# Optimization experiments

Measured on AMD Instinct MI355X. Metric: run time of the kernel, lower is better.

Reference implementation:

```python
import jax, jax.numpy as jnp
import numpy as np

N = 8192
IN_F = 256
OUT_F = 128


def setup_inputs() -> dict:
    key = jax.random.key(0)
    k1, k2, k3, k4, k5, k6 = jax.random.split(key, 6)
    input = jax.random.normal(k1, (N, IN_F), dtype=jnp.float32)
    adj = jax.random.randint(k2, (N, N), 0, 2, dtype=jnp.int32)
    # xavier-uniform-like init scaled by gain=0.5
    def xavier(k, shape, gain=0.5):
        fan_in, fan_out = shape[0], shape[1]
        lim = gain * np.sqrt(6.0 / (fan_in + fan_out))
        return jax.random.uniform(k, shape, dtype=jnp.float32, minval=-lim, maxval=lim)
    W_s = xavier(k3, (IN_F, OUT_F))
    a_s = xavier(k4, (OUT_F, 1))
    W_n = xavier(k5, (IN_F, OUT_F))
    a_n = xavier(k6, (OUT_F, 1))
    return {"input": input, "adj": adj, "W_s": W_s, "a_s": a_s, "W_n": W_n, "a_n": a_n}


def reference(input, adj, W_s, a_s, W_n, a_n):
    # Projections: [N, out_features]
    h_s = input @ W_s
    h_n = input @ W_n
    # Additive attention logits: e[i, j] = relu((h_s @ a_s)[i] + (h_n @ a_n)[j])
    e = jax.nn.relu((h_s @ a_s) + (h_n @ a_n).T)  # [N, N]
    # Masked softmax over neighbors (dim=1)
    attention = jnp.where(adj > 0, e, jnp.float32(-9e15))
    attention = jax.nn.softmax(attention, axis=1)
    # Self-scaling term (sum of softmax rows, kept for faithfulness)
    attention_sum = jnp.sum(attention, axis=-1, keepdims=True)
    attention_s = 1.0 / (1.0 + attention_sum)
    # Dropout is identity in eval mode (p=0 / training=False)
    h_prime = attention_s * h_s + attention @ h_n
    # concat=True -> elu activation
    return jax.nn.elu(h_prime)
```

## Files before the change

### kernel.cpp

```cpp
#include <hip/hip_runtime.h>
#include <math.h>

#define NN 8192

typedef short short8 __attribute__((ext_vector_type(8)));
typedef float f32x4 __attribute__((ext_vector_type(4)));

__device__ __forceinline__ float eluf(float x) {
  return x > 0.f ? x : (__expf(x) - 1.f);
}
__device__ __forceinline__ unsigned short f2bf(float f) {
  union { float f; unsigned u; } v; v.f = f;
  unsigned r = v.u + 0x7fffu + ((v.u >> 16) & 1u);
  return (unsigned short)(r >> 16);
}
__device__ __forceinline__ unsigned pack4(int4 v, int sh) {
  return ((unsigned)(v.x & 1) << sh) | ((unsigned)(v.y & 1) << (sh + 1)) |
         ((unsigned)(v.z & 1) << (sh + 2)) | ((unsigned)(v.w & 1) << (sh + 3));
}

__global__ __launch_bounds__(256) void k_proj(const float* __restrict__ X,
                                              const float* __restrict__ Ws,
                                              const float* __restrict__ Wn,
                                              const float* __restrict__ as_,
                                              const float* __restrict__ an_,
                                              float* __restrict__ Hs,
                                              unsigned short* __restrict__ HnT,
                                              float* __restrict__ es_out,
                                              float* __restrict__ en_out) {
  __shared__ float4 lin4[8 * 64];
  const int t = threadIdx.x;
  const int i0 = blockIdx.x * 8;
  const float4* Xg = (const float4*)X + (size_t)i0 * 64;
  lin4[t] = Xg[t];
  if (t < 256) lin4[t + 256] = Xg[t + 256];
  __syncthreads();
  const int c = t & 127;
  const int rh = t >> 7;
  float accs[4], accn[4];
#pragma unroll
  for (int r = 0; r < 4; ++r) { accs[r] = 0.f; accn[r] = 0.f; }
  for (int k = 0; k < 256; k += 4) {
    float ws0 = Ws[(k + 0) * 128 + c], ws1 = Ws[(k + 1) * 128 + c];
    float ws2 = Ws[(k + 2) * 128 + c], ws3 = Ws[(k + 3) * 128 + c];
    float wn0 = Wn[(k + 0) * 128 + c], wn1 = Wn[(k + 1) * 128 + c];
    float wn2 = Wn[(k + 2) * 128 + c], wn3 = Wn[(k + 3) * 128 + c];
#pragma unroll
    for (int r = 0; r < 4; ++r) {
      float4 iv = lin4[(rh * 4 + r) * 64 + (k >> 2)];
      accs[r] = fmaf(iv.x, ws0, accs[r]); accs[r] = fmaf(iv.y, ws1, accs[r]);
      accs[r] = fmaf(iv.z, ws2, accs[r]); accs[r] = fmaf(iv.w, ws3, accs[r]);
      accn[r] = fmaf(iv.x, wn0, accn[r]); accn[r] = fmaf(iv.y, wn1, accn[r]);
      accn[r] = fmaf(iv.z, wn2, accn[r]); accn[r] = fmaf(iv.w, wn3, accn[r]);
    }
  }
#pragma unroll
  for (int r = 0; r < 4; ++r)
    Hs[(size_t)(i0 + rh * 4 + r) * 128 + c] = accs[r];
  {
    union { unsigned short us[4]; ushort4 u4; } pk;
#pragma unroll
    for (int r = 0; r < 4; ++r) pk.us[r] = f2bf(accn[r]);
    *(ushort4*)(HnT + (size_t)blockIdx.x * 1024 + c * 8 + rh * 4) = pk.u4;
  }
  float* red = (float*)lin4;
  const int wv = t >> 6, ln = t & 63;
  __syncthreads();
  {
    float av = as_[c];
#pragma unroll
    for (int r = 0; r < 4; ++r) red[(rh * 4 + r) * 128 + c] = accs[r] * av;
  }
  __syncthreads();
#pragma unroll
  for (int h = 0; h < 2; ++h) {
    int row = wv * 2 + h;
    float p = red[row * 128 + ln] + red[row * 128 + 64 + ln];
#pragma unroll
    for (int off = 32; off >= 1; off >>= 1) p += __shfl_down(p, off);
    if (ln == 0) es_out[i0 + row] = __expf(p);
  }
  __syncthreads();
  {
    float av = an_[c];
#pragma unroll
    for (int r = 0; r < 4; ++r) red[(rh * 4 + r) * 128 + c] = accn[r] * av;
  }
  __syncthreads();
#pragma unroll
  for (int h = 0; h < 2; ++h) {
    int row = wv * 2 + h;
    float p = red[row * 128 + ln] + red[row * 128 + 64 + ln];
#pragma unroll
    for (int off = 32; off >= 1; off >>= 1) p += __shfl_down(p, off);
    if (ln == 0) en_out[i0 + row] = __expf(p);
  }
}

__global__ __launch_bounds__(512, 4) void k_main(const int* __restrict__ A,
                                                 const unsigned short* __restrict__ HnT,
                                                 const float* __restrict__ es_g,
                                                 const float* __restrict__ en_g,
                                                 float* __restrict__ HsOut) {
  __shared__ __align__(16) char smem[49152];
  float* en_lds = (float*)smem;
  unsigned* bits_lds = (unsigned*)(smem + 32768);
  float* cmb = (float*)smem;
  __shared__ float zsh[8][16];
  __shared__ float zf[16];

  const int t = threadIdx.x;
  const int wv = t >> 6;
  const int ln = t & 63;
  const int q = ln >> 4;
  const int m = ln & 15;
  const int row0 = blockIdx.x * 16;

  {
    float4* dst = (float4*)en_lds;
    const float4* s4 = (const float4*)en_g;
#pragma unroll
    for (int k = 0; k < 4; ++k) dst[t + k * 512] = s4[t + k * 512];
#pragma unroll 1
    for (int k = 0; k < 8; ++k) {
      int g = t + k * 512;
      int rr = g >> 8;
      int c8 = g & 255;
      const int4* src = (const int4*)(A + (size_t)(row0 + rr) * NN + c8 * 32);
      int4 v0 = src[0], v1 = src[1], v2 = src[2], v3 = src[3];
      int4 v4 = src[4], v5 = src[5], v6 = src[6], v7 = src[7];
      unsigned w = pack4(v0, 0)  | pack4(v1, 4)  | pack4(v2, 8)  | pack4(v3, 12) |
                   pack4(v4, 16) | pack4(v5, 20) | pack4(v6, 24) | pack4(v7, 28);
      bits_lds[(c8 >> 5) * 512 + (c8 & 31) * 16 + rr] = w;
    }
  }

  const float sme = es_g[row0 + m];
  const unsigned short* bptr = HnT + ((size_t)(wv * 128 + q) * 128 + m) * 8;
  const float* nvl = en_lds + wv * 1024 + q * 8;
  const unsigned* bts = bits_lds + wv * 512 + m;

  f32x4 acc[8];
#pragma unroll
  for (int ft = 0; ft < 8; ++ft) acc[ft] = (f32x4){0.f, 0.f, 0.f, 0.f};
  float zp = 0.f;

  union Breg { uint4 u; short8 s; };
  Breg breg[8];

  __syncthreads();

  breg[0].u = *(const uint4*)(bptr);       breg[1].u = *(const uint4*)(bptr + 128);
  breg[2].u = *(const uint4*)(bptr + 256); breg[3].u = *(const uint4*)(bptr + 384);
  breg[4].u = *(const uint4*)(bptr + 512); breg[5].u = *(const uint4*)(bptr + 640);
  breg[6].u = *(const uint4*)(bptr + 768); breg[7].u = *(const uint4*)(bptr + 896);

#pragma unroll 2
  for (int tt = 0; tt < 32; ++tt) {
    short8 fr;
    {
      float4 nv0 = *(const float4*)(nvl + tt * 32);
      float4 nv1 = *(const float4*)(nvl + tt * 32 + 4);
      const unsigned bw = bts[tt * 16];
      const unsigned byte = (bw >> (q * 8)) & 0xffu;
      float ev[8] = {nv0.x, nv0.y, nv0.z, nv0.w, nv1.x, nv1.y, nv1.z, nv1.w};
#pragma unroll
      for (int k = 0; k < 8; ++k) {
        float w = ((byte >> k) & 1u) ? fmaxf(sme * ev[k], 1.f) : 0.f;
        zp += w;
        fr[k] = (short)f2bf(w);
      }
    }
    __builtin_amdgcn_s_setprio(1);
    acc[0] = __builtin_amdgcn_mfma_f32_16x16x32_bf16(fr, breg[0].s, acc[0], 0, 0, 0);
    acc[1] = __builtin_amdgcn_mfma_f32_16x16x32_bf16(fr, breg[1].s, acc[1], 0, 0, 0);
    acc[2] = __builtin_amdgcn_mfma_f32_16x16x32_bf16(fr, breg[2].s, acc[2], 0, 0, 0);
    acc[3] = __builtin_amdgcn_mfma_f32_16x16x32_bf16(fr, breg[3].s, acc[3], 0, 0, 0);
    acc[4] = __builtin_amdgcn_mfma_f32_16x16x32_bf16(fr, breg[4].s, acc[4], 0, 0, 0);
    acc[5] = __builtin_amdgcn_mfma_f32_16x16x32_bf16(fr, breg[5].s, acc[5], 0, 0, 0);
    acc[6] = __builtin_amdgcn_mfma_f32_16x16x32_bf16(fr, breg[6].s, acc[6], 0, 0, 0);
    acc[7] = __builtin_amdgcn_mfma_f32_16x16x32_bf16(fr, breg[7].s, acc[7], 0, 0, 0);
    __builtin_amdgcn_s_setprio(0);
    {
      const unsigned short* p = bptr + (size_t)(tt + 1) * 4096;
      breg[0].u = *(const uint4*)(p);       breg[1].u = *(const uint4*)(p + 128);
      breg[2].u = *(const uint4*)(p + 256); breg[3].u = *(const uint4*)(p + 384);
      breg[4].u = *(const uint4*)(p + 512); breg[5].u = *(const uint4*)(p + 640);
      breg[6].u = *(const uint4*)(p + 768); breg[7].u = *(const uint4*)(p + 896);
    }
  }

  {
    float zz = zp;
    zz += __shfl_down(zz, 32);
    zz += __shfl_down(zz, 16);
    if (ln < 16) zsh[wv][ln] = zz;
  }
  __syncthreads();
  if (wv >= 4) {
#pragma unroll
    for (int ft = 0; ft < 8; ++ft)
#pragma unroll
      for (int reg = 0; reg < 4; ++reg)
        cmb[(wv - 4) * 2048 + (q * 4 + reg) * 128 + ft * 16 + m] = acc[ft][reg];
  }
  __syncthreads();
  if (wv < 4) {
#pragma unroll
    for (int ft = 0; ft < 8; ++ft)
#pragma unroll
      for (int reg = 0; reg < 4; ++reg)
        acc[ft][reg] += cmb[wv * 2048 + (q * 4 + reg) * 128 + ft * 16 + m];
  }
  __syncthreads();
  if (wv < 4) {
#pragma unroll
    for (int ft = 0; ft < 8; ++ft)
#pragma unroll
      for (int reg = 0; reg < 4; ++reg)
        cmb[wv * 2048 + (q * 4 + reg) * 128 + ft * 16 + m] = acc[ft][reg];
  }
  if (t < 16) {
    float z = zsh[0][t] + zsh[1][t] + zsh[2][t] + zsh[3][t] +
              zsh[4][t] + zsh[5][t] + zsh[6][t] + zsh[7][t];
    zf[t] = 1.f / z;
  }
  __syncthreads();
  {
    const int row = t >> 5;
    const int f0 = (t & 31) * 4;
    f32x4 ssum = *(const f32x4*)&cmb[row * 128 + f0];
#pragma unroll
    for (int w = 1; w < 4; ++w) ssum += *(const f32x4*)&cmb[w * 2048 + row * 128 + f0];
    const float invz = zf[row];
    const size_t off = (size_t)(row0 + row) * 128 + f0;
    float4 h = *(const float4*)(HsOut + off);
    float4 o;
    o.x = eluf(fmaf(ssum[0], invz, 0.5f * h.x));
    o.y = eluf(fmaf(ssum[1], invz, 0.5f * h.y));
    o.z = eluf(fmaf(ssum[2], invz, 0.5f * h.z));
    o.w = eluf(fmaf(ssum[3], invz, 0.5f * h.w));
    *(float4*)(HsOut + off) = o;
  }
}

extern "C" void kernel_launch(void* const* d_in, const int* in_sizes, int n_in,
                              void* d_out, int out_size, void* d_ws, size_t ws_size,
                              hipStream_t stream) {
  const float* X   = (const float*)d_in[0];
  const int*   A   = (const int*)d_in[1];
  const float* Ws  = (const float*)d_in[2];
  const float* as_ = (const float*)d_in[3];
  const float* Wn  = (const float*)d_in[4];
  const float* an_ = (const float*)d_in[5];
  float* out = (float*)d_out;

  unsigned short* HnT = (unsigned short*)d_ws;
  float* es = (float*)(HnT + (size_t)128 * NN);
  float* en = es + NN;

  k_proj<<<1024, 256, 0, stream>>>(X, Ws, Wn, as_, an_, out, HnT, es, en);
  k_main<<<512, 512, 0, stream>>>(A, HnT, es, en, out);
}
```

Baseline: 423.7 us.

## Pack adjacency bitmask in a separate pre-pass fused with projection kernel

Adjacency-to-bitmask packing moves from the attention kernel's prologue into the projection kernel, run as extra interleaved blocks that write a packed bit array to workspace. The main kernel then reads 32x less adjacency data per block before its compute loop. This removes the long serialized global-load prologue from each main block. The cost is an extra write and read of the packed mask and a larger first kernel.

Result: no change. 418.3 us (-1.3%).

```diff
diff --git a/kernel.cpp b/kernel.cpp
--- a/kernel.cpp
+++ b/kernel.cpp
@@ -19,21 +19,43 @@
          ((unsigned)(v.z & 1) << (sh + 2)) | ((unsigned)(v.w & 1) << (sh + 3));
 }
 
-__global__ __launch_bounds__(256) void k_proj(const float* __restrict__ X,
-                                              const float* __restrict__ Ws,
-                                              const float* __restrict__ Wn,
-                                              const float* __restrict__ as_,
-                                              const float* __restrict__ an_,
-                                              float* __restrict__ Hs,
-                                              unsigned short* __restrict__ HnT,
-                                              float* __restrict__ es_out,
-                                              float* __restrict__ en_out) {
+__global__ __launch_bounds__(256) void k_pre(const float* __restrict__ X,
+                                             const int* __restrict__ A,
+                                             const float* __restrict__ Ws,
+                                             const float* __restrict__ Wn,
+                                             const float* __restrict__ as_,
+                                             const float* __restrict__ an_,
+                                             float* __restrict__ Hs,
+                                             unsigned short* __restrict__ HnT,
+                                             float* __restrict__ es_out,
+                                             float* __restrict__ en_out,
+                                             unsigned* __restrict__ P) {
   __shared__ float4 lin4[8 * 64];
+  const int bid = blockIdx.x;
+  const int q5 = bid / 5, r5 = bid - q5 * 5;
   const int t = threadIdx.x;
-  const int i0 = blockIdx.x * 8;
+
+  if (r5 == 4) {
+    const int row0 = q5 * 32;
+#pragma unroll 1
+    for (int k = 0; k < 32; ++k) {
+      int g = t + k * 256;
+      int rr = g >> 8;
+      int c8 = g & 255;
+      const int4* src = (const int4*)(A + (size_t)(row0 + rr) * NN + c8 * 32);
+      int4 v0 = src[0], v1 = src[1], v2 = src[2], v3 = src[3];
+      int4 v4 = src[4], v5 = src[5], v6 = src[6], v7 = src[7];
+      unsigned w = pack4(v0, 0)  | pack4(v1, 4)  | pack4(v2, 8)  | pack4(v3, 12) |
+                   pack4(v4, 16) | pack4(v5, 20) | pack4(v6, 24) | pack4(v7, 28);
+      P[(size_t)(row0 + rr) * 256 + c8] = w;
+    }
+    return;
+  }
+
+  const int i0 = (q5 * 4 + r5) * 8;
   const float4* Xg = (const float4*)X + (size_t)i0 * 64;
   lin4[t] = Xg[t];
-  if (t < 256) lin4[t + 256] = Xg[t + 256];
+  lin4[t + 256] = Xg[t + 256];
   __syncthreads();
   const int c = t & 127;
   const int rh = t >> 7;
@@ -61,7 +83,7 @@
     union { unsigned short us[4]; ushort4 u4; } pk;
 #pragma unroll
     for (int r = 0; r < 4; ++r) pk.us[r] = f2bf(accn[r]);
-    *(ushort4*)(HnT + (size_t)blockIdx.x * 1024 + c * 8 + rh * 4) = pk.u4;
+    *(ushort4*)(HnT + (size_t)(i0 >> 3) * 1024 + c * 8 + rh * 4) = pk.u4;
   }
   float* red = (float*)lin4;
   const int wv = t >> 6, ln = t & 63;
@@ -97,7 +119,7 @@
   }
 }
 
-__global__ __launch_bounds__(512, 4) void k_main(const int* __restrict__ A,
+__global__ __launch_bounds__(512, 4) void k_main(const unsigned* __restrict__ Pk,
                                                  const unsigned short* __restrict__ HnT,
                                                  const float* __restrict__ es_g,
                                                  const float* __restrict__ en_g,
@@ -121,16 +143,12 @@
     const float4* s4 = (const float4*)en_g;
 #pragma unroll
     for (int k = 0; k < 4; ++k) dst[t + k * 512] = s4[t + k * 512];
-#pragma unroll 1
+#pragma unroll
     for (int k = 0; k < 8; ++k) {
       int g = t + k * 512;
       int rr = g >> 8;
       int c8 = g & 255;
-      const int4* src = (const int4*)(A + (size_t)(row0 + rr) * NN + c8 * 32);
-      int4 v0 = src[0], v1 = src[1], v2 = src[2], v3 = src[3];
-      int4 v4 = src[4], v5 = src[5], v6 = src[6], v7 = src[7];
-      unsigned w = pack4(v0, 0)  | pack4(v1, 4)  | pack4(v2, 8)  | pack4(v3, 12) |
-                   pack4(v4, 16) | pack4(v5, 20) | pack4(v6, 24) | pack4(v7, 28);
+      unsigned w = Pk[(size_t)(row0 + rr) * 256 + c8];
       bits_lds[(c8 >> 5) * 512 + (c8 & 31) * 16 + rr] = w;
     }
   }
@@ -258,7 +276,8 @@
   unsigned short* HnT = (unsigned short*)d_ws;
   float* es = (float*)(HnT + (size_t)128 * NN);
   float* en = es + NN;
-
-  k_proj<<<1024, 256, 0, stream>>>(X, Ws, Wn, as_, an_, out, HnT, es, en);
-  k_main<<<512, 512, 0, stream>>>(A, HnT, es, en, out);
-}
+  unsigned* P = (unsigned*)(en + NN);
+
+  k_pre<<<1280, 256, 0, stream>>>(X, A, Ws, Wn, as_, an_, out, HnT, es, en, P);
+  k_main<<<512, 512, 0, stream>>>(P, HnT, es, en, out);
+}
```
